# Kernel optimization log

Measured on AMD Instinct MI355X. Metric: run time of the kernel, lower is better.

The kernel has to match this reference:

```python
import jax, jax.numpy as jnp
import numpy as np

# NTM copy-task constants (from ntm_reproduction)
B, T, IN = 2048, 66, 9          # batch, total timesteps, bits+delimiter
H = 100                          # controller LSTM units
N, D = 128, 20                   # memory slots, memory vector dim
OUT = 8                          # output bits
CLIP = 20.0
NUM_HEADS = 2                    # 1 read + 1 write head
PPH = D + 1 + 1 + 3 + 1          # k, beta, g, s(3), gamma = 26 params per head
EPS = 1e-8


def setup_inputs() -> dict:
    key = jax.random.key(0)
    ks = jax.random.split(key, 8)
    s = 0.1
    ctrl_in = IN + D  # input concat with prev read vector
    return {
        "inputs": jax.random.uniform(ks[0], (B, T, IN), dtype=jnp.float32),
        "Wx": jax.random.normal(ks[1], (ctrl_in, 4 * H), dtype=jnp.float32) * s,
        "Wh": jax.random.normal(ks[2], (H, 4 * H), dtype=jnp.float32) * s,
        "b_lstm": jnp.zeros((4 * H,), jnp.float32),
        "W_params": jax.random.normal(ks[3], (H, NUM_HEADS * PPH + 2 * D), dtype=jnp.float32) * s,
        "b_params": jnp.zeros((NUM_HEADS * PPH + 2 * D,), jnp.float32),
        "W_out": jax.random.normal(ks[4], (H + D, OUT), dtype=jnp.float32) * s,
        "b_out": jnp.zeros((OUT,), jnp.float32),
        "sequence_length": 32,
    }


def _ntm_forward(inputs, Wx, Wh, b_lstm, W_params, b_params, W_out, b_out):
    Bt = inputs.shape[0]

    def step(carry, x_t):
        h, c, r, w_prev, M = carry  # w_prev: [B,2,N], M: [B,N,D]
        # --- controller LSTM ---
        ctrl = jnp.concatenate([x_t, r], axis=-1)
        gates = ctrl @ Wx + h @ Wh + b_lstm
        i, f, g, o = jnp.split(gates, 4, axis=-1)
        c = jax.nn.sigmoid(f) * c + jax.nn.sigmoid(i) * jnp.tanh(g)
        h = jax.nn.sigmoid(o) * jnp.tanh(c)
        # --- head parameters ---
        p = jnp.clip(h @ W_params + b_params, -CLIP, CLIP)
        hp = p[:, : NUM_HEADS * PPH].reshape(Bt, NUM_HEADS, PPH)
        k = jnp.tanh(hp[..., :D])                        # [B,2,D]
        beta = jax.nn.softplus(hp[..., D])               # [B,2]
        gg = jax.nn.sigmoid(hp[..., D + 1])              # [B,2]
        s_sh = jax.nn.softmax(hp[..., D + 2 : D + 5], axis=-1)  # [B,2,3]
        gamma = jax.nn.softplus(hp[..., D + 5]) + 1.0    # [B,2]
        # --- content addressing: cosine similarity ---
        kn = jnp.linalg.norm(k, axis=-1, keepdims=True)          # [B,2,1]
        Mn = jnp.linalg.norm(M, axis=-1)                         # [B,N]
        cos = jnp.einsum('bhd,bnd->bhn', k, M) / (kn * Mn[:, None, :] + EPS)
        w_c = jax.nn.softmax(beta[..., None] * cos, axis=-1)     # [B,2,N]
        # --- interpolation gate ---
        w_g = gg[..., None] * w_c + (1.0 - gg[..., None]) * w_prev
        # --- circular convolution shift (shifts -1, 0, +1) ---
        w_t = (s_sh[..., 0:1] * jnp.roll(w_g, -1, axis=-1)
               + s_sh[..., 1:2] * w_g
               + s_sh[..., 2:3] * jnp.roll(w_g, 1, axis=-1))
        # --- sharpening ---
        w_pow = jnp.power(jnp.maximum(w_t, 1e-16), gamma[..., None])
        w = w_pow / jnp.sum(w_pow, axis=-1, keepdims=True)       # [B,2,N]
        w_r, w_w = w[:, 0], w[:, 1]
        # --- read (from pre-write memory) ---
        r_new = jnp.einsum('bn,bnd->bd', w_r, M)
        # --- write: erase then add ---
        e = jax.nn.sigmoid(p[:, NUM_HEADS * PPH : NUM_HEADS * PPH + D])  # [B,D]
        a = jnp.tanh(p[:, NUM_HEADS * PPH + D :])                         # [B,D]
        M = M * (1.0 - w_w[..., None] * e[:, None, :]) + w_w[..., None] * a[:, None, :]
        # --- output ---
        out = jnp.clip(jnp.concatenate([h, r_new], axis=-1) @ W_out + b_out, -CLIP, CLIP)
        return (h, c, r_new, w, M), out

    h0 = jnp.zeros((Bt, H), inputs.dtype)
    c0 = jnp.zeros((Bt, H), inputs.dtype)
    r0 = jnp.zeros((Bt, D), inputs.dtype)
    w0 = jnp.zeros((Bt, NUM_HEADS, N), inputs.dtype).at[:, :, 0].set(1.0)
    M0 = jnp.full((Bt, N, D), 1e-6, inputs.dtype)
    _, outs = jax.lax.scan(step, (h0, c0, r0, w0, M0), jnp.swapaxes(inputs, 0, 1))
    return jnp.swapaxes(outs, 0, 1)  # [B,T,OUT]


def reference(inputs, Wx, Wh, b_lstm, W_params, b_params, W_out, b_out, sequence_length):
    logits = _ntm_forward(inputs, Wx, Wh, b_lstm, W_params, b_params, W_out, b_out)
    return jax.nn.sigmoid(logits[:, sequence_length + 1 :, :])
```

## Files before the change

kernel.cpp:

```cpp
#include <hip/hip_runtime.h>

namespace {

constexpr int B_TOT  = 2048;
constexpr int T_SEQ  = 66;
constexpr int IN_DIM = 9;
constexpr int H      = 100;
constexpr int N      = 128;
constexpr int D      = 20;
constexpr int G      = 4;
constexpr int NTHR   = 512;
constexpr float CLIPV = 20.0f;

constexpr int NCT_SM  = 25;
constexpr int WS_BIG_SLOTS = 32 * 4 * 64;
constexpr int WS_SM_OFF_U16 = WS_BIG_SLOTS * 8;
constexpr int WS_SM_SLOTS = NCT_SM * 64;

constexpr int MT_ROW = 132;
constexpr int MSKT   = D * MT_ROW + 4;

constexpr int HA_STRIDE = 160;
constexpr int HA_LO     = 4 * HA_STRIDE;
constexpr int HA_TOT    = 8 * HA_STRIDE;
constexpr int SA_STRIDE = 32;
constexpr int SA_TOT    = 4 * SA_STRIDE;
constexpr int W_ROW = 132;

constexpr int OFF_M    = 0;
constexpr int OFF_GT   = OFF_M + G * MSKT;
constexpr int OFF_C    = OFF_GT + 2048;
constexpr int OFF_HA   = OFF_C + 400;
constexpr int OFF_SA   = OFF_HA + HA_TOT / 2;
constexpr int OFF_BIAS = OFF_SA + SA_TOT / 2;
constexpr int OFF_R    = OFF_BIAS + 512;
constexpr int OFF_KV   = OFF_R + 80;
constexpr int OFF_SC   = OFF_KV + 160;
constexpr int OFF_EA   = OFF_SC + 64;
constexpr int OFF_W    = OFF_EA + 160;
constexpr int OFF_WO2  = OFF_W + 8 * W_ROW;
constexpr int OFF_OUT  = OFF_WO2 + 160;
constexpr int SMEM_FLOATS = OFF_OUT + 1152;
constexpr int SMEM_BYTES  = SMEM_FLOATS * 4;

typedef __attribute__((ext_vector_type(8))) short bf16x8;
typedef __attribute__((ext_vector_type(4))) float f32x4;

__device__ __forceinline__ float fexp2(float x) { return __builtin_amdgcn_exp2f(x); }
__device__ __forceinline__ float flog2(float x) { return __builtin_amdgcn_logf(x); }
__device__ __forceinline__ float frcp(float x)  { return __builtin_amdgcn_rcpf(x); }
__device__ __forceinline__ float fexp(float x)  { return fexp2(x * 1.4426950408889634f); }
__device__ __forceinline__ float fsig(float x)  { return frcp(1.f + fexp2(-1.4426950408889634f * x)); }
__device__ __forceinline__ float ftanh(float x) { return 1.f - 2.f * frcp(1.f + fexp2(2.8853900817779268f * x)); }
__device__ __forceinline__ float fsoftplus(float x) { return log1pf(fexp(x)); }

__device__ __forceinline__ unsigned short f2bf(float x) {
  unsigned u = __float_as_uint(x);
  u = (u + 0x7FFFu + ((u >> 16) & 1u)) >> 16;
  return (unsigned short)u;
}
__device__ __forceinline__ float bf2f(unsigned short h) {
  return __uint_as_float(((unsigned)h) << 16);
}

template <int C>
__device__ __forceinline__ float dpp_add(float x) {
  return x + __int_as_float(__builtin_amdgcn_mov_dpp(__float_as_int(x), C, 0xF, 0xF, true));
}
__device__ __forceinline__ float qred(float x) { return dpp_add<0x4E>(dpp_add<0xB1>(x)); }

__device__ __forceinline__ void wred_max2(float& a, float& b) {
#pragma unroll
  for (int off = 32; off; off >>= 1) {
    a = fmaxf(a, __shfl_xor(a, off, 64));
    b = fmaxf(b, __shfl_xor(b, off, 64));
  }
}
__device__ __forceinline__ void wred_sum2(float& a, float& b) {
#pragma unroll
  for (int off = 32; off; off >>= 1) {
    a += __shfl_xor(a, off, 64);
    b += __shfl_xor(b, off, 64);
  }
}

__global__ void setup_kernel(unsigned short* __restrict__ ws,
                             const float* __restrict__ Wx, const float* __restrict__ Wh,
                             const float* __restrict__ Wp, const float* __restrict__ Wo) {
  int idx = blockIdx.x * 256 + threadIdx.x;
  if (idx < WS_BIG_SLOTS) {
    int lane = idx & 63, kt = (idx >> 6) & 3, ct = idx >> 8;
    int col = ct * 16 + (lane & 15);
    int k0 = kt * 32 + ((lane >> 4) << 3);
    unsigned short v[8];
#pragma unroll
    for (int j = 0; j < 8; ++j) {
      int k = k0 + j;
      float f = 0.f;
      if (k < 100) {
        if (col < 400) f = Wh[k * 400 + col];
        else if (col < 492) f = Wp[k * 92 + (col - 400)];
        else if (col < 500) f = Wo[k * 8 + (col - 492)];
      }
      v[j] = f2bf(f);
    }
    uint4 pk;
    pk.x = (unsigned)v[0] | ((unsigned)v[1] << 16);
    pk.y = (unsigned)v[2] | ((unsigned)v[3] << 16);
    pk.z = (unsigned)v[4] | ((unsigned)v[5] << 16);
    pk.w = (unsigned)v[6] | ((unsigned)v[7] << 16);
    *(uint4*)(ws + (size_t)idx * 8) = pk;
  } else if (idx < WS_BIG_SLOTS + WS_SM_SLOTS) {
    int s = idx - WS_BIG_SLOTS;
    int lane = s & 63, ct = s >> 6;
    int col = ct * 16 + (lane & 15);
    int k0 = (lane >> 4) << 3;
    unsigned short v[8];
#pragma unroll
    for (int j = 0; j < 8; ++j) {
      int k = k0 + j;
      float f = (k < 29) ? Wx[k * 400 + col] : 0.f;
      v[j] = f2bf(f);
    }
    uint4 pk;
    pk.x = (unsigned)v[0] | ((unsigned)v[1] << 16);
    pk.y = (unsigned)v[2] | ((unsigned)v[3] << 16);
    pk.z = (unsigned)v[4] | ((unsigned)v[5] << 16);
    pk.w = (unsigned)v[6] | ((unsigned)v[7] << 16);
    *(uint4*)(ws + (size_t)(WS_SM_OFF_U16 + (size_t)s * 8)) = pk;
  }
}

__global__ __launch_bounds__(NTHR, 4) void ntm_kernel(
    const float* __restrict__ inputs, const unsigned short* __restrict__ wsu,
    const float* __restrict__ b_lstm, const float* __restrict__ b_params,
    const float* __restrict__ b_out, const float* __restrict__ W_out,
    const int* __restrict__ seqp, float* __restrict__ outp) {
  extern __shared__ float sm[];
  const int tid = threadIdx.x;
  const int lane = tid & 63;
  const int wv = tid >> 6;
  const int b0 = blockIdx.x * G;
  const int tlim = seqp[0] + 1;
  const int TO = T_SEQ - tlim;
  const bool buffered = (TO <= 36);
  unsigned short* hAu = (unsigned short*)(sm + OFF_HA);
  unsigned short* sAu = (unsigned short*)(sm + OFF_SA);
  const bf16x8* wsBig = (const bf16x8*)wsu;
  const bf16x8* wsSm  = (const bf16x8*)(wsu + WS_SM_OFF_U16);

  for (int i = tid; i < G * MSKT; i += NTHR) sm[OFF_M + i] = 1e-6f;
  for (int i = tid; i < 2048; i += NTHR) sm[OFF_GT + i] = 0.f;
  for (int i = tid; i < 400; i += NTHR) sm[OFF_C + i] = 0.f;
  for (int i = tid; i < HA_TOT; i += NTHR) hAu[i] = 0;
  for (int i = tid; i < SA_TOT; i += NTHR) sAu[i] = 0;
  if (tid < 512) {
    float v = 0.f;
    if (tid < 400) v = b_lstm[tid];
    else if (tid < 492) v = b_params[tid - 400];
    else if (tid < 500) v = b_out[tid - 492];
    sm[OFF_BIAS + tid] = v;
  }
  for (int i = tid; i < 80; i += NTHR) sm[OFF_R + i] = 0.f;
  for (int i = tid; i < 8 * W_ROW; i += NTHR)
    sm[OFF_W + i] = ((i % W_ROW) == 0) ? 1.f : 0.f;
  for (int i = tid; i < 160; i += NTHR) sm[OFF_WO2 + i] = W_out[800 + i];
  for (int i = tid; i < 1152; i += NTHR) sm[OFF_OUT + i] = 0.f;
  if (tid >= 448 && tid < 484) {
    int p = tid - 448, g = p / 9, k = p - g * 9;
    sAu[g * SA_STRIDE + k] = f2bf(inputs[(size_t)(b0 + g) * T_SEQ * IN_DIM + k]);
  }
  __syncthreads();

  const int arow = lane & 3;
  const int akoff = (lane >> 4) << 3;

  if (wv < 7) {
    bf16x8 as = *(const bf16x8*)(sAu + arow * SA_STRIDE + akoff);
#pragma unroll
    for (int cti = 0; cti < 4; ++cti) {
      int ct = wv * 4 + cti;
      if (ct < NCT_SM) {
        float bv = sm[OFF_BIAS + ct * 16 + (lane & 15)];
        f32x4 a = {bv, bv, bv, bv};
        a = __builtin_amdgcn_mfma_f32_16x16x32_bf16(as, wsSm[ct * 64 + lane], a, 0, 0, 0);
        if (lane < 16) *(f32x4*)&sm[OFF_GT + (ct * 16 + lane) * 4] = a;
      }
    }
  }
  __syncthreads();

  for (int t = 0; t < T_SEQ; ++t) {
    if (tid < 400) {
      int e = tid >> 2, g = tid & 3;
      float gi = sm[OFF_GT + e * 4 + g];
      float gf = sm[OFF_GT + (100 + e) * 4 + g];
      float gz = sm[OFF_GT + (200 + e) * 4 + g];
      float go = sm[OFF_GT + (300 + e) * 4 + g];
      float c = sm[OFF_C + e * 4 + g];
      float nc = fsig(gf) * c + fsig(gi) * ftanh(gz);
      float h = fsig(go) * ftanh(nc);
      sm[OFF_C + e * 4 + g] = nc;
      unsigned short hh = f2bf(h);
      unsigned short hl = f2bf(h - bf2f(hh));
      hAu[g * HA_STRIDE + e] = hh;
      hAu[HA_LO + g * HA_STRIDE + e] = hl;
    } else if (tid >= 416 && tid < 452) {
      if (t + 1 < T_SEQ) {
        int p = tid - 416, g = p / 9, k = p - g * 9;
        sAu[g * SA_STRIDE + k] =
            f2bf(inputs[((size_t)(b0 + g) * T_SEQ + (t + 1)) * IN_DIM + k]);
      }
    } else if (tid >= 456 && tid < 488) {
      int s = t - 1;
      if (s >= tlim) {
        int u = tid - 456, g = u >> 3, o = u & 7;
        float v = sm[OFF_GT + (492 + o) * 4 + g];
#pragma unroll
        for (int d = 0; d < D; ++d)
          v = fmaf(sm[OFF_R + d * 4 + g], sm[OFF_WO2 + d * 8 + o], v);
        v = fminf(fmaxf(v, -CLIPV), CLIPV);
        v = fsig(v);
        int tp = s - tlim;
        if (buffered) sm[OFF_OUT + (g * TO + tp) * 8 + o] = v;
        else outp[((size_t)(b0 + g) * TO + tp) * 8 + o] = v;
      }
    }
    __syncthreads();

    if (wv < 7) {
      const int ct = 25 + wv;
      float bv = sm[OFF_BIAS + ct * 16 + (lane & 15)];
      f32x4 a = {bv, bv, bv, bv};
#pragma unroll
      for (int kt = 0; kt < 4; ++kt) {
        bf16x8 ahi = *(const bf16x8*)(hAu + arow * HA_STRIDE + kt * 32 + akoff);
        bf16x8 alo = *(const bf16x8*)(hAu + HA_LO + arow * HA_STRIDE + kt * 32 + akoff);
        bf16x8 bf = wsBig[(ct * 4 + kt) * 64 + lane];
        a = __builtin_amdgcn_mfma_f32_16x16x32_bf16(ahi, bf, a, 0, 0, 0);
        a = __builtin_amdgcn_mfma_f32_16x16x32_bf16(alo, bf, a, 0, 0, 0);
      }
      if (lane < 16) {
        int col = ct * 16 + lane;
        if (col < 492) {
          a.x = fminf(fmaxf(a.x, -CLIPV), CLIPV);
          a.y = fminf(fmaxf(a.y, -CLIPV), CLIPV);
          a.z = fminf(fmaxf(a.z, -CLIPV), CLIPV);
          a.w = fminf(fmaxf(a.w, -CLIPV), CLIPV);
        }
        *(f32x4*)&sm[OFF_GT + col * 4] = a;
      }
    }
    __syncthreads();

    if (wv < 4) {
      const int g = wv, l = lane;
      if (l < 40) {
        int hd = l >= 20, j = l - 20 * hd;
        sm[OFF_KV + (2 * g + hd) * 20 + j] =
            ftanh(sm[OFF_GT + (400 + hd * 26 + j) * 4 + g]);
      } else if (l < 52) {
        int hd = (l - 40) >= 6, which = (l - 40) - 6 * hd;
        float v = sm[OFF_GT + (400 + hd * 26 + 20 + which) * 4 + g];
        float* scp = &sm[OFF_SC + (2 * g + hd) * 8];
        if (which == 0) scp[0] = fsoftplus(v);
        else if (which == 1) scp[1] = fsig(v);
        else if (which == 2) {
          float a1 = sm[OFF_GT + (400 + hd * 26 + 23) * 4 + g];
          float a2 = sm[OFF_GT + (400 + hd * 26 + 24) * 4 + g];
          float mx = fmaxf(v, fmaxf(a1, a2));
          float e0 = fexp(v - mx), e1 = fexp(a1 - mx), e2 = fexp(a2 - mx);
          float inv = frcp(e0 + e1 + e2);
          scp[2] = e0 * inv; scp[3] = e1 * inv; scp[4] = e2 * inv;
        } else if (which == 5) {
          scp[5] = fsoftplus(v) + 1.f;
        }
      }
      asm volatile("s_waitcnt lgkmcnt(0)" ::: "memory");
      __builtin_amdgcn_sched_barrier(0);

      const float* Mg = &sm[OFF_M + g * MSKT];
      const float* kv0 = &sm[OFF_KV + (2 * g) * 20];
      const float* kv1 = &sm[OFF_KV + (2 * g + 1) * 20];
      float d00 = 0.f, d01 = 0.f, d10 = 0.f, d11 = 0.f;
      float kn0 = 0.f, kn1 = 0.f, n0s = 0.f, n1s = 0.f;
#pragma unroll
      for (int d = 0; d < D; ++d) {
        float k0 = kv0[d], k1 = kv1[d];
        float m0 = Mg[d * MT_ROW + l], m1 = Mg[d * MT_ROW + 64 + l];
        d00 = fmaf(k0, m0, d00); d01 = fmaf(k0, m1, d01);
        d10 = fmaf(k1, m0, d10); d11 = fmaf(k1, m1, d11);
        kn0 = fmaf(k0, k0, kn0); kn1 = fmaf(k1, k1, kn1);
        n0s = fmaf(m0, m0, n0s); n1s = fmaf(m1, m1, n1s);
      }
      kn0 = sqrtf(kn0); kn1 = sqrtf(kn1);
      float Mn0 = sqrtf(n0s), Mn1 = sqrtf(n1s);
      const float* sc0 = &sm[OFF_SC + (2 * g) * 8];
      const float* sc1 = &sm[OFF_SC + (2 * g + 1) * 8];
      float be0 = sc0[0], be1 = sc1[0];
      float S00 = be0 * d00 * frcp(kn0 * Mn0 + 1e-8f);
      float S01 = be0 * d01 * frcp(kn0 * Mn1 + 1e-8f);
      float S10 = be1 * d10 * frcp(kn1 * Mn0 + 1e-8f);
      float S11 = be1 * d11 * frcp(kn1 * Mn1 + 1e-8f);
      float mx0 = fmaxf(S00, S01), mx1 = fmaxf(S10, S11);
      wred_max2(mx0, mx1);
      float e00 = fexp(S00 - mx0), e01 = fexp(S01 - mx0);
      float e10 = fexp(S10 - mx1), e11 = fexp(S11 - mx1);
      float sum0 = e00 + e01, sum1 = e10 + e11;
      wred_sum2(sum0, sum1);
      float si0 = frcp(sum0), si1 = frcp(sum1);
      float* wpa = &sm[OFF_W + (2 * g) * W_ROW];
      float* wpb = &sm[OFF_W + (2 * g + 1) * W_ROW];
      float gg0 = sc0[1], gg1 = sc1[1];
      float wa0 = wpa[l], wa1 = wpa[64 + l], wb0 = wpb[l], wb1 = wpb[64 + l];
      float wg00 = fmaf(gg0, e00 * si0 - wa0, wa0);
      float wg01 = fmaf(gg0, e01 * si0 - wa1, wa1);
      float wg10 = fmaf(gg1, e10 * si1 - wb0, wb0);
      float wg11 = fmaf(gg1, e11 * si1 - wb1, wb1);
      int lp = (l + 1) & 63, lm = (l + 63) & 63;
      float n00 = __shfl(wg00, lp, 64), n01 = __shfl(wg01, lp, 64);
      float p00 = __shfl(wg00, lm, 64), p01 = __shfl(wg01, lm, 64);
      float a0l0 = __shfl(wg00, 0, 64), a1l0 = __shfl(wg01, 0, 64);
      float a0l63 = __shfl(wg00, 63, 64), a1l63 = __shfl(wg01, 63, 64);
      float nxt00 = (l == 63) ? a1l0 : n00;
      float nxt01 = (l == 63) ? a0l0 : n01;
      float prv00 = (l == 0) ? a1l63 : p00;
      float prv01 = (l == 0) ? a0l63 : p01;
      float n10 = __shfl(wg10, lp, 64), n11 = __shfl(wg11, lp, 64);
      float p10 = __shfl(wg10, lm, 64), p11 = __shfl(wg11, lm, 64);
      float b0l0 = __shfl(wg10, 0, 64), b1l0 = __shfl(wg11, 0, 64);
      float b0l63 = __shfl(wg10, 63, 64), b1l63 = __shfl(wg11, 63, 64);
      float nxt10 = (l == 63) ? b1l0 : n10;
      float nxt11 = (l == 63) ? b0l0 : n11;
      float prv10 = (l == 0) ? b1l63 : p10;
      float prv11 = (l == 0) ? b0l63 : p11;
      float s00 = sc0[2], s01s = sc0[3], s02 = sc0[4], gm0 = sc0[5];
      float s10 = sc1[2], s11s = sc1[3], s12 = sc1[4], gm1 = sc1[5];
      float wt00 = fmaxf(fmaf(s00, nxt00, fmaf(s01s, wg00, s02 * prv00)), 1e-16f);
      float wt01 = fmaxf(fmaf(s00, nxt01, fmaf(s01s, wg01, s02 * prv01)), 1e-16f);
      float wt10 = fmaxf(fmaf(s10, nxt10, fmaf(s11s, wg10, s12 * prv10)), 1e-16f);
      float wt11 = fmaxf(fmaf(s10, nxt11, fmaf(s11s, wg11, s12 * prv11)), 1e-16f);
      float m0m = fmaxf(wt00, wt01), m1m = fmaxf(wt10, wt11);
      wred_max2(m0m, m1m);
      float iv0 = frcp(m0m), iv1 = frcp(m1m);
      float q00 = fexp2(gm0 * flog2(wt00 * iv0));
      float q01 = fexp2(gm0 * flog2(wt01 * iv0));
      float q10 = fexp2(gm1 * flog2(wt10 * iv1));
      float q11 = fexp2(gm1 * flog2(wt11 * iv1));
      float sq0 = q00 + q01, sq1 = q10 + q11;
      wred_sum2(sq0, sq1);
      float pi0 = frcp(sq0), pi1 = frcp(sq1);
      wpa[l] = q00 * pi0; wpa[64 + l] = q01 * pi0;
      wpb[l] = q10 * pi1; wpb[64 + l] = q11 * pi1;
    } else {
      const int wq = wv - 4;
      bf16x8 ahi[4], alo[4];
#pragma unroll
      for (int kt = 0; kt < 4; ++kt) {
        ahi[kt] = *(const bf16x8*)(hAu + arow * HA_STRIDE + kt * 32 + akoff);
        alo[kt] = *(const bf16x8*)(hAu + HA_LO + arow * HA_STRIDE + kt * 32 + akoff);
      }
#pragma unroll
      for (int cti = 0; cti < 7; ++cti) {
        int ct = wq + cti * 4;
        if (ct < NCT_SM) {
          float bv = sm[OFF_BIAS + ct * 16 + (lane & 15)];
          f32x4 a = {bv, bv, bv, bv};
#pragma unroll
          for (int kt = 0; kt < 4; ++kt) {
            bf16x8 bf = wsBig[(ct * 4 + kt) * 64 + lane];
            a = __builtin_amdgcn_mfma_f32_16x16x32_bf16(ahi[kt], bf, a, 0, 0, 0);
            a = __builtin_amdgcn_mfma_f32_16x16x32_bf16(alo[kt], bf, a, 0, 0, 0);
          }
          if (lane < 16) *(f32x4*)&sm[OFF_GT + (ct * 16 + lane) * 4] = a;
        }
      }
    }
    __syncthreads();

    if (tid < 320) {
      int pr = tid >> 2, nq = tid & 3;
      int g = pr / 20, d = pr - g * 20;
      const float* wr = &sm[OFF_W + (2 * g) * W_ROW];
      const float* Md = &sm[OFF_M + g * MSKT + d * MT_ROW];
      float s = 0.f;
#pragma unroll
      for (int i = 0; i < 8; ++i) {
        int n = nq * 4 + i * 16;
        float4 w4 = *(const float4*)(wr + n);
        float4 m4 = *(const float4*)(Md + n);
        s = fmaf(w4.x, m4.x, fmaf(w4.y, m4.y, fmaf(w4.z, m4.z, fmaf(w4.w, m4.w, s))));
      }
      s = qred(s);
      if (nq == 0) {
        sm[OFF_R + d * 4 + g] = s;
        sAu[g * SA_STRIDE + 9 + d] = f2bf(s);
      }
    } else if (tid < 480) {
      int p = tid - 320, g = p / 40, j = p - g * 40;
      float v = sm[OFF_GT + (452 + j) * 4 + g];
      sm[OFF_EA + g * 40 + j] = (j < 20) ? fsig(v) : ftanh(v);
    }
    __syncthreads();

    if (wv < 7) {
      bf16x8 as = *(const bf16x8*)(sAu + arow * SA_STRIDE + akoff);
#pragma unroll
      for (int cti = 0; cti < 4; ++cti) {
        int ct = wv * 4 + cti;
        if (ct < NCT_SM) {
          bf16x8 bs = wsSm[ct * 64 + lane];
          f32x4 c = *(const f32x4*)&sm[OFF_GT + (ct * 16 + (lane & 15)) * 4];
          c = __builtin_amdgcn_mfma_f32_16x16x32_bf16(as, bs, c, 0, 0, 0);
          if (lane < 16) *(f32x4*)&sm[OFF_GT + (ct * 16 + lane) * 4] = c;
        }
      }
    }
    if (tid < 256) {
      int g = tid >> 6, n0 = tid & 63;
      const float* ep = &sm[OFF_EA + g * 40];
      const float* ap = ep + 20;
      float* Mg = &sm[OFF_M + g * MSKT];
#pragma unroll
      for (int h2 = 0; h2 < 2; ++h2) {
        int n = n0 + 64 * h2;
        float ww = sm[OFF_W + (2 * g + 1) * W_ROW + n];
#pragma unroll
        for (int d = 0; d < D; ++d) {
          float mv = Mg[d * MT_ROW + n];
          Mg[d * MT_ROW + n] = fmaf(ww, fmaf(-ep[d], mv, ap[d]), mv);
        }
      }
    }
    __syncthreads();
  }

  if (tid < 32) {
    int s = T_SEQ - 1;
    if (s >= tlim) {
      int g = tid >> 3, o = tid & 7;
      float v = sm[OFF_GT + (492 + o) * 4 + g];
#pragma unroll
      for (int d = 0; d < D; ++d)
        v = fmaf(sm[OFF_R + d * 4 + g], sm[OFF_WO2 + d * 8 + o], v);
      v = fminf(fmaxf(v, -CLIPV), CLIPV);
      v = fsig(v);
      int tp = s - tlim;
      if (buffered) sm[OFF_OUT + (g * TO + tp) * 8 + o] = v;
      else outp[((size_t)(b0 + g) * TO + tp) * 8 + o] = v;
    }
  }
  __syncthreads();
  if (buffered) {
    const int total = G * TO * 8;
    for (int i = tid * 4; i < total; i += NTHR * 4) {
      float4 v = *(const float4*)&sm[OFF_OUT + i];
      *(float4*)&outp[(size_t)blockIdx.x * total + i] = v;
    }
  }
}

}

extern "C" void kernel_launch(void* const* d_in, const int* in_sizes, int n_in,
                              void* d_out, int out_size, void* d_ws, size_t ws_size,
                              hipStream_t stream) {
  (void)in_sizes; (void)n_in; (void)out_size; (void)ws_size;
  const float* inputs   = (const float*)d_in[0];
  const float* Wx       = (const float*)d_in[1];
  const float* Wh       = (const float*)d_in[2];
  const float* b_lstm   = (const float*)d_in[3];
  const float* W_params = (const float*)d_in[4];
  const float* b_params = (const float*)d_in[5];
  const float* W_out    = (const float*)d_in[6];
  const float* b_out    = (const float*)d_in[7];
  const int*   seqp     = (const int*)d_in[8];
  float* out = (float*)d_out;
  unsigned short* wsu = (unsigned short*)d_ws;

  constexpr int SETUP_N = WS_BIG_SLOTS + WS_SM_SLOTS;
  setup_kernel<<<(SETUP_N + 255) / 256, 256, 0, stream>>>(wsu, Wx, Wh, W_params,
                                                          W_out);

  hipFuncSetAttribute((const void*)ntm_kernel,
                      hipFuncAttributeMaxDynamicSharedMemorySize, SMEM_BYTES);
  ntm_kernel<<<B_TOT / G, NTHR, SMEM_BYTES, stream>>>(
      inputs, wsu, b_lstm, b_params, b_out, W_out, seqp, out);
}
```

Measured before the change: 559.6 us.

## Defer memory write into param-GEMM phase, cache row norms, use DPP reductions

The memory erase/add update moves out of the end of each step and into the next step's head-parameter MFMA phase. Warps 4-7 now run it while warps 0-3 handle the seven column tiles, two tiles per warp. During the update the per-slot memory row norms are computed and stored in shared memory, so the cosine-similarity phase reads them instead of recomputing them. The wave-wide max and sum reductions use DPP moves for the intra-row steps and keep shuffles only for the 16 and 32 offsets. The cost is extra shared memory and less MFMA parallelism, since four warps now do the work seven did.

```diff
diff --git a/kernel.cpp b/kernel.cpp
--- a/kernel.cpp
+++ b/kernel.cpp
@@ -37,7 +37,8 @@
 constexpr int OFF_KV   = OFF_R + 80;
 constexpr int OFF_SC   = OFF_KV + 160;
 constexpr int OFF_EA   = OFF_SC + 64;
-constexpr int OFF_W    = OFF_EA + 160;
+constexpr int OFF_MN   = OFF_EA + 160;
+constexpr int OFF_W    = OFF_MN + 512;
 constexpr int OFF_WO2  = OFF_W + 8 * W_ROW;
 constexpr int OFF_OUT  = OFF_WO2 + 160;
 constexpr int SMEM_FLOATS = OFF_OUT + 1152;
@@ -64,24 +65,28 @@
 }
 
 template <int C>
-__device__ __forceinline__ float dpp_add(float x) {
-  return x + __int_as_float(__builtin_amdgcn_mov_dpp(__float_as_int(x), C, 0xF, 0xF, true));
-}
+__device__ __forceinline__ float dpp_mov(float x) {
+  return __int_as_float(__builtin_amdgcn_mov_dpp(__float_as_int(x), C, 0xF, 0xF, true));
+}
+template <int C>
+__device__ __forceinline__ float dpp_add(float x) { return x + dpp_mov<C>(x); }
 __device__ __forceinline__ float qred(float x) { return dpp_add<0x4E>(dpp_add<0xB1>(x)); }
 
 __device__ __forceinline__ void wred_max2(float& a, float& b) {
-#pragma unroll
-  for (int off = 32; off; off >>= 1) {
-    a = fmaxf(a, __shfl_xor(a, off, 64));
-    b = fmaxf(b, __shfl_xor(b, off, 64));
-  }
+  a = fmaxf(a, dpp_mov<0xB1>(a));  b = fmaxf(b, dpp_mov<0xB1>(b));
+  a = fmaxf(a, dpp_mov<0x4E>(a));  b = fmaxf(b, dpp_mov<0x4E>(b));
+  a = fmaxf(a, dpp_mov<0x124>(a)); b = fmaxf(b, dpp_mov<0x124>(b));
+  a = fmaxf(a, dpp_mov<0x128>(a)); b = fmaxf(b, dpp_mov<0x128>(b));
+  a = fmaxf(a, __shfl_xor(a, 16, 64)); b = fmaxf(b, __shfl_xor(b, 16, 64));
+  a = fmaxf(a, __shfl_xor(a, 32, 64)); b = fmaxf(b, __shfl_xor(b, 32, 64));
 }
 __device__ __forceinline__ void wred_sum2(float& a, float& b) {
-#pragma unroll
-  for (int off = 32; off; off >>= 1) {
-    a += __shfl_xor(a, off, 64);
-    b += __shfl_xor(b, off, 64);
-  }
+  a = dpp_add<0xB1>(a);  b = dpp_add<0xB1>(b);
+  a = dpp_add<0x4E>(a);  b = dpp_add<0x4E>(b);
+  a = dpp_add<0x124>(a); b = dpp_add<0x124>(b);
+  a = dpp_add<0x128>(a); b = dpp_add<0x128>(b);
+  a += __shfl_xor(a, 16, 64); b += __shfl_xor(b, 16, 64);
+  a += __shfl_xor(a, 32, 64); b += __shfl_xor(b, 32, 64);
 }
 
 __global__ void setup_kernel(unsigned short* __restrict__ ws,
@@ -162,6 +167,7 @@
     sm[OFF_BIAS + tid] = v;
   }
   for (int i = tid; i < 80; i += NTHR) sm[OFF_R + i] = 0.f;
+  for (int i = tid; i < 512; i += NTHR) sm[OFF_MN + i] = 4.47213595e-6f;
   for (int i = tid; i < 8 * W_ROW; i += NTHR)
     sm[OFF_W + i] = ((i % W_ROW) == 0) ? 1.f : 0.f;
   for (int i = tid; i < 160; i += NTHR) sm[OFF_WO2 + i] = W_out[800 + i];
@@ -228,27 +234,56 @@
     }
     __syncthreads();
 
-    if (wv < 7) {
-      const int ct = 25 + wv;
-      float bv = sm[OFF_BIAS + ct * 16 + (lane & 15)];
-      f32x4 a = {bv, bv, bv, bv};
+    if (wv < 4) {
+      bf16x8 ahi[4], alo[4];
 #pragma unroll
       for (int kt = 0; kt < 4; ++kt) {
-        bf16x8 ahi = *(const bf16x8*)(hAu + arow * HA_STRIDE + kt * 32 + akoff);
-        bf16x8 alo = *(const bf16x8*)(hAu + HA_LO + arow * HA_STRIDE + kt * 32 + akoff);
-        bf16x8 bf = wsBig[(ct * 4 + kt) * 64 + lane];
-        a = __builtin_amdgcn_mfma_f32_16x16x32_bf16(ahi, bf, a, 0, 0, 0);
-        a = __builtin_amdgcn_mfma_f32_16x16x32_bf16(alo, bf, a, 0, 0, 0);
-      }
-      if (lane < 16) {
-        int col = ct * 16 + lane;
-        if (col < 492) {
-          a.x = fminf(fmaxf(a.x, -CLIPV), CLIPV);
-          a.y = fminf(fmaxf(a.y, -CLIPV), CLIPV);
-          a.z = fminf(fmaxf(a.z, -CLIPV), CLIPV);
-          a.w = fminf(fmaxf(a.w, -CLIPV), CLIPV);
+        ahi[kt] = *(const bf16x8*)(hAu + arow * HA_STRIDE + kt * 32 + akoff);
+        alo[kt] = *(const bf16x8*)(hAu + HA_LO + arow * HA_STRIDE + kt * 32 + akoff);
+      }
+#pragma unroll
+      for (int rep = 0; rep < 2; ++rep) {
+        int ct = 25 + wv + rep * 4;
+        if (ct < 32) {
+          float bv = sm[OFF_BIAS + ct * 16 + (lane & 15)];
+          f32x4 a = {bv, bv, bv, bv};
+#pragma unroll
+          for (int kt = 0; kt < 4; ++kt) {
+            bf16x8 bf = wsBig[(ct * 4 + kt) * 64 + lane];
+            a = __builtin_amdgcn_mfma_f32_16x16x32_bf16(ahi[kt], bf, a, 0, 0, 0);
+            a = __builtin_amdgcn_mfma_f32_16x16x32_bf16(alo[kt], bf, a, 0, 0, 0);
+          }
+          if (lane < 16) {
+            int col = ct * 16 + lane;
+            if (col < 492) {
+              a.x = fminf(fmaxf(a.x, -CLIPV), CLIPV);
+              a.y = fminf(fmaxf(a.y, -CLIPV), CLIPV);
+              a.z = fminf(fmaxf(a.z, -CLIPV), CLIPV);
+              a.w = fminf(fmaxf(a.w, -CLIPV), CLIPV);
+            }
+            *(f32x4*)&sm[OFF_GT + col * 4] = a;
+          }
         }
-        *(f32x4*)&sm[OFF_GT + col * 4] = a;
+      }
+    } else if (t > 0) {
+      int slot = tid - 256;
+      int g = slot >> 6, n0 = slot & 63;
+      const float* ep = &sm[OFF_EA + g * 40];
+      const float* ap = ep + 20;
+      float* Mg = &sm[OFF_M + g * MSKT];
+#pragma unroll
+      for (int h2 = 0; h2 < 2; ++h2) {
+        int n = n0 + 64 * h2;
+        float ww = sm[OFF_W + (2 * g + 1) * W_ROW + n];
+        float nrm = 0.f;
+#pragma unroll
+        for (int d = 0; d < D; ++d) {
+          float mv = Mg[d * MT_ROW + n];
+          mv = fmaf(ww, fmaf(-ep[d], mv, ap[d]), mv);
+          Mg[d * MT_ROW + n] = mv;
+          nrm = fmaf(mv, mv, nrm);
+        }
+        sm[OFF_MN + g * N + n] = sqrtf(nrm);
       }
     }
     __syncthreads();
@@ -283,7 +318,7 @@
       const float* kv0 = &sm[OFF_KV + (2 * g) * 20];
       const float* kv1 = &sm[OFF_KV + (2 * g + 1) * 20];
       float d00 = 0.f, d01 = 0.f, d10 = 0.f, d11 = 0.f;
-      float kn0 = 0.f, kn1 = 0.f, n0s = 0.f, n1s = 0.f;
+      float kn0 = 0.f, kn1 = 0.f;
 #pragma unroll
       for (int d = 0; d < D; ++d) {
         float k0 = kv0[d], k1 = kv1[d];
@@ -291,10 +326,10 @@
         d00 = fmaf(k0, m0, d00); d01 = fmaf(k0, m1, d01);
         d10 = fmaf(k1, m0, d10); d11 = fmaf(k1, m1, d11);
         kn0 = fmaf(k0, k0, kn0); kn1 = fmaf(k1, k1, kn1);
-        n0s = fmaf(m0, m0, n0s); n1s = fmaf(m1, m1, n1s);
       }
       kn0 = sqrtf(kn0); kn1 = sqrtf(kn1);
-      float Mn0 = sqrtf(n0s), Mn1 = sqrtf(n1s);
+      float Mn0 = sm[OFF_MN + g * N + l];
+      float Mn1 = sm[OFF_MN + g * N + 64 + l];
       const float* sc0 = &sm[OFF_SC + (2 * g) * 8];
       const float* sc1 = &sm[OFF_SC + (2 * g + 1) * 8];
       float be0 = sc0[0], be1 = sc1[0];
@@ -416,22 +451,6 @@
         }
       }
     }
-    if (tid < 256) {
-      int g = tid >> 6, n0 = tid & 63;
-      const float* ep = &sm[OFF_EA + g * 40];
-      const float* ap = ep + 20;
-      float* Mg = &sm[OFF_M + g * MSKT];
-#pragma unroll
-      for (int h2 = 0; h2 < 2; ++h2) {
-        int n = n0 + 64 * h2;
-        float ww = sm[OFF_W + (2 * g + 1) * W_ROW + n];
-#pragma unroll
-        for (int d = 0; d < D; ++d) {
-          float mv = Mg[d * MT_ROW + n];
-          Mg[d * MT_ROW + n] = fmaf(ww, fmaf(-ep[d], mv, ap[d]), mv);
-        }
-      }
-    }
     __syncthreads();
   }
 
```

Measured after the change: 588.0 us. +5.1%, slower.
